# Performance work log

Hardware: AMD Instinct MI355X
Metric: run time of the kernel (lower is better)

## Reference

```python
import jax, jax.numpy as jnp
import numpy as np

DEPTH, HEADS, K, EPS = 4, 8, 3, 1e-5
DIM, CIN, COUT = 128, 64, 64


def conv1x1(x, w, b=None):
    y = jnp.einsum('oi,bihw->bohw', w, x)
    return y if b is None else y + b[None, :, None, None]


def dilated_conv3x3(x, w, b, d):
    y = jax.lax.conv_general_dilated(
        x, w, window_strides=(1, 1), padding=[(d, d), (d, d)],
        rhs_dilation=(d, d), dimension_numbers=('NCHW', 'OIHW', 'NCHW'))
    return y + b[None, :, None, None]


def batchnorm_train(x, g, b):
    # BatchNorm2d in training mode: biased batch stats over (B,H,W)
    mu = jnp.mean(x, axis=(0, 2, 3), keepdims=True)
    var = jnp.var(x, axis=(0, 2, 3), keepdims=True)
    return (x - mu) * jax.lax.rsqrt(var + EPS) * g[None, :, None, None] + b[None, :, None, None]


def unfold3(x):
    # nn.Unfold(k=3, pad=1): (B,C,H,W) -> (B,C,k*k,H,W), patch index row-major (dy,dx)
    B, C, H, W = x.shape
    p = K // 2
    xp = jnp.pad(x, ((0, 0), (0, 0), (p, p), (p, p)))
    return jnp.stack([xp[:, :, dy:dy + H, dx:dx + W]
                      for dy in range(K) for dx in range(K)], axis=2)


def local_self_attention(x, qkv_w, fc_w, fc_b):
    B, C, H, W = x.shape
    c = C // HEADS
    scale = c ** -0.5
    qkv = conv1x1(x, qkv_w)                      # (B,3C,H,W)
    q, k, v = jnp.split(qkv, 3, axis=1)
    shape6 = lambda t: unfold3(t).reshape(B, HEADS, c, K * K, H, W)
    q, k, v = shape6(q) * scale, shape6(k), shape6(v)
    # NOTE: original einsum labels dim2 (channels/head) as n/m and dim3 (k^2) as the
    # contracted axis, i.e. channel-attention contracted over the 9 patch positions.
    dots = jnp.einsum('bhnkij,bhmkij->bhnmij', q, k)   # (B,h,c,c,H,W)
    attn = jax.nn.softmax(dots, axis=3)
    out = jnp.einsum('bhnmij,bhmkij->bhnkij', attn, v)  # (B,h,c,k^2,H,W)
    out = out.reshape(B, C, K * K, H, W).sum(axis=2)
    return conv1x1(out, fc_w, fc_b) + x


def setup_inputs() -> dict:
    key = jax.random.key(0)
    ks = jax.random.split(key, 12)
    s = 0.05
    return {
        'x': jax.random.normal(ks[0], (2, CIN, 96, 96), jnp.float32),
        'w_in': jax.random.normal(ks[1], (DIM, CIN), jnp.float32) * s,
        'b_in': jnp.zeros((DIM,), jnp.float32),
        'conv_w': jax.random.normal(ks[2], (DEPTH, DIM, DIM, 3, 3), jnp.float32) * s,
        'conv_b': jnp.zeros((DEPTH, DIM), jnp.float32),
        'bn_g': jnp.ones((DEPTH, DIM), jnp.float32),
        'bn_b': jnp.zeros((DEPTH, DIM), jnp.float32),
        'qkv_w': jax.random.normal(ks[3], (DEPTH, 3 * DIM, DIM), jnp.float32) * s,
        'fc_w': jax.random.normal(ks[4], (DEPTH, DIM, DIM), jnp.float32) * s,
        'fc_b': jnp.zeros((DEPTH, DIM), jnp.float32),
        'w_out': jax.random.normal(ks[5], (COUT, DIM), jnp.float32) * s,
        'b_out': jnp.zeros((COUT,), jnp.float32),
    }


def reference(x, w_in, b_in, conv_w, conv_b, bn_g, bn_b, qkv_w, fc_w, fc_b, w_out, b_out):
    h = conv1x1(x, w_in, b_in)
    for i in range(DEPTH):
        d = 2 ** i
        h = jax.nn.relu(batchnorm_train(dilated_conv3x3(h, conv_w[i], conv_b[i], d), bn_g[i], bn_b[i]))
        h = local_self_attention(h, qkv_w[i], fc_w[i], fc_b[i])
    return conv1x1(h, w_out, b_out)
```

## Files before the change

### kernel.cpp

```cpp
#include <hip/hip_runtime.h>
#include <math.h>

typedef __attribute__((ext_vector_type(8))) short bf16x8;
typedef __attribute__((ext_vector_type(4))) float f32x4;
typedef __attribute__((ext_vector_type(4))) unsigned short us4;
typedef __attribute__((ext_vector_type(8))) unsigned short us8;

constexpr int BB = 2;
constexpr int CC = 128;
constexpr int HH = 96, WW = 96;
constexpr int PP = HH * WW;
constexpr int NN = BB * PP;
constexpr size_t PLANE_F = (size_t)NN * CC;

__device__ __forceinline__ float bf2f(unsigned short u) {
    return __uint_as_float(((unsigned)u) << 16);
}
__device__ __forceinline__ unsigned short f2bf(float f) {
    unsigned u = __float_as_uint(f);
    unsigned r = u + 0x7fff + ((u >> 16) & 1);
    return (unsigned short)(r >> 16);
}

__global__ __launch_bounds__(256)
void k_wconv(const float* __restrict__ conv_w, const float* __restrict__ qkv_w,
             const float* __restrict__ fc_w, const float* __restrict__ w_in,
             const float* __restrict__ w_out,
             unsigned short* __restrict__ wcv, unsigned short* __restrict__ wqkv,
             unsigned short* __restrict__ wfc, unsigned short* __restrict__ wi,
             unsigned short* __restrict__ wo)
{
    int gid = blockIdx.x * 256 + threadIdx.x;
    if (gid < 589824) {
        int L = gid / 147456, r = gid % 147456;
        int o = r / 1152, k = r % 1152;
        int t = k / 128, c = k % 128;
        float v = conv_w[(((size_t)(L * 128 + o) * 128 + c) * 9) + t];
        wcv[gid] = f2bf(v);
    } else if (gid < 786432) {
        int g = gid - 589824;
        int o = (g % 49152) / 128;
        float v = qkv_w[g] * (o < 128 ? 0.25f : 1.0f);
        wqkv[g] = f2bf(v);
    } else if (gid < 851968) {
        int g = gid - 786432;
        wfc[g] = f2bf(fc_w[g]);
    } else if (gid < 860160) {
        int g = gid - 851968;
        wi[g] = f2bf(w_in[g]);
    } else if (gid < 868352) {
        int g = gid - 860160;
        wo[g] = f2bf(w_out[g]);
    }
}

__global__ __launch_bounds__(256)
void k_xconv(const float* __restrict__ x, unsigned short* __restrict__ xT)
{
    int n = blockIdx.x * 256 + threadIdx.x;
    int b = n / PP, p = n - b * PP;
    unsigned short* dst = xT + (size_t)n * 64;
    #pragma unroll
    for (int cg = 0; cg < 16; ++cg) {
        us4 st;
        #pragma unroll
        for (int r = 0; r < 4; ++r)
            st[r] = f2bf(x[((size_t)(b * 64 + cg * 4 + r)) * PP + p]);
        *reinterpret_cast<us4*>(dst + cg * 4) = st;
    }
}

template<int WM, int WN, int MODE, int DIL>
__global__ __launch_bounds__(WM * WN * 64)
void k_gemm(const unsigned short* __restrict__ W,
            const unsigned short* __restrict__ act,
            const float* __restrict__ bias,
            const unsigned short* __restrict__ resid,
            void* __restrict__ outp,
            const unsigned short* __restrict__ zp,
            int Kw, int Cin, int Cout)
{
    int tid = threadIdx.x;
    int lane = tid & 63, wv = tid >> 6;
    int wm = wv % WM, wn = wv / WM;
    int l15 = lane & 15, kg = lane >> 4;

    int n_base = blockIdx.x * (WN * 96) + wn * 96;
    int o_base = blockIdx.y * (WM * 64) + wm * 64;

    const unsigned short* wbase[4];
    #pragma unroll
    for (int fm = 0; fm < 4; ++fm) {
        int o = o_base + fm * 16 + l15;
        wbase[fm] = W + (size_t)o * Kw + kg * 8;
    }

    const unsigned short* bbase[6];
    int iF[6], jF[6];
    #pragma unroll
    for (int fn = 0; fn < 6; ++fn) {
        int n = n_base + fn * 16 + l15;
        bbase[fn] = act + (size_t)n * Cin + kg * 8;
        if (DIL > 0) {
            int pix = n % PP;
            iF[fn] = pix / WW;
            jF[fn] = pix % WW;
        }
    }

    f32x4 acc[4][6];
    #pragma unroll
    for (int fm = 0; fm < 4; ++fm)
        #pragma unroll
        for (int fn = 0; fn < 6; ++fn)
            acc[fm][fn] = (f32x4){0.f, 0.f, 0.f, 0.f};

    if constexpr (DIL > 0) {
        const unsigned short* zpk = zp + kg * 8;
        int t0 = blockIdx.z * 3;
        for (int t = t0; t < t0 + 3; ++t) {
            int oy = (t / 3 - 1) * DIL, ox = (t % 3 - 1) * DIL;
            int disp = (oy * WW + ox) * Cin;
            const unsigned short* baddr[6];
            #pragma unroll
            for (int fn = 0; fn < 6; ++fn) {
                bool v = ((unsigned)(iF[fn] + oy) < (unsigned)HH) &&
                         ((unsigned)(jF[fn] + ox) < (unsigned)WW);
                baddr[fn] = v ? (bbase[fn] + disp) : zpk;
            }
            #pragma unroll
            for (int c0 = 0; c0 < 128; c0 += 32) {
                bf16x8 a[4], b[6];
                #pragma unroll
                for (int fm = 0; fm < 4; ++fm)
                    a[fm] = *reinterpret_cast<const bf16x8*>(wbase[fm] + t * 128 + c0);
                #pragma unroll
                for (int fn = 0; fn < 6; ++fn)
                    b[fn] = *reinterpret_cast<const bf16x8*>(baddr[fn] + c0);
                #pragma unroll
                for (int fm = 0; fm < 4; ++fm)
                    #pragma unroll
                    for (int fn = 0; fn < 6; ++fn)
                        acc[fm][fn] = __builtin_amdgcn_mfma_f32_16x16x32_bf16(
                            a[fm], b[fn], acc[fm][fn], 0, 0, 0);
            }
        }
    } else {
        #pragma unroll
        for (int k0 = 0; k0 < 128; k0 += 32) {
            if (k0 >= Cin) break;
            bf16x8 a[4], b[6];
            #pragma unroll
            for (int fm = 0; fm < 4; ++fm)
                a[fm] = *reinterpret_cast<const bf16x8*>(wbase[fm] + k0);
            #pragma unroll
            for (int fn = 0; fn < 6; ++fn)
                b[fn] = *reinterpret_cast<const bf16x8*>(bbase[fn] + k0);
            #pragma unroll
            for (int fm = 0; fm < 4; ++fm)
                #pragma unroll
                for (int fn = 0; fn < 6; ++fn)
                    acc[fm][fn] = __builtin_amdgcn_mfma_f32_16x16x32_bf16(
                        a[fm], b[fn], acc[fm][fn], 0, 0, 0);
        }
    }

    #pragma unroll
    for (int fm = 0; fm < 4; ++fm) {
        #pragma unroll
        for (int fn = 0; fn < 6; ++fn) {
            f32x4 v = acc[fm][fn];
            int n = n_base + fn * 16 + l15;
            int o0 = o_base + fm * 16 + kg * 4;
            if constexpr (MODE == 1) {
                float* op = (float*)outp + (size_t)blockIdx.z * PLANE_F;
                *reinterpret_cast<f32x4*>(op + (size_t)n * Cout + o0) = v;
            } else if constexpr (MODE == 0 || MODE == 2) {
                if (bias) {
                    #pragma unroll
                    for (int r = 0; r < 4; ++r) v[r] += bias[o0 + r];
                }
                if constexpr (MODE == 2) {
                    us4 rv = *reinterpret_cast<const us4*>(resid + (size_t)n * Cout + o0);
                    #pragma unroll
                    for (int r = 0; r < 4; ++r) v[r] += bf2f(rv[r]);
                }
                us4 st;
                #pragma unroll
                for (int r = 0; r < 4; ++r) st[r] = f2bf(v[r]);
                *reinterpret_cast<us4*>((unsigned short*)outp + (size_t)n * Cout + o0) = st;
            } else {
                int b_ = n / PP, p = n - b_ * PP;
                float* op = (float*)outp;
                #pragma unroll
                for (int r = 0; r < 4; ++r)
                    op[((size_t)(b_ * Cout + o0 + r)) * PP + p] = v[r] + bias[o0 + r];
            }
        }
    }
}

__global__ __launch_bounds__(256)
void k_bnpart(const float* __restrict__ y, float* __restrict__ partials)
{
    int t = threadIdx.x;
    int cq = t & 31, ng = t >> 5;
    int n0 = blockIdx.x * 384 + ng * 48;
    f32x4 s = {0.f, 0.f, 0.f, 0.f}, s2 = {0.f, 0.f, 0.f, 0.f};
    for (int r = 0; r < 48; ++r) {
        size_t idx = (size_t)(n0 + r) * CC + cq * 4;
        f32x4 a = *reinterpret_cast<const f32x4*>(y + idx);
        f32x4 b = *reinterpret_cast<const f32x4*>(y + PLANE_F + idx);
        f32x4 c = *reinterpret_cast<const f32x4*>(y + 2 * PLANE_F + idx);
        #pragma unroll
        for (int e = 0; e < 4; ++e) {
            float v = a[e] + b[e] + c[e];
            s[e] += v; s2[e] += v * v;
        }
    }
    __shared__ f32x4 ls[256], ls2[256];
    ls[t] = s; ls2[t] = s2;
    __syncthreads();
    if (t < 32) {
        f32x4 S = ls[t], S2 = ls2[t];
        #pragma unroll
        for (int g = 1; g < 8; ++g) {
            f32x4 a = ls[g * 32 + t], b = ls2[g * 32 + t];
            #pragma unroll
            for (int e = 0; e < 4; ++e) { S[e] += a[e]; S2[e] += b[e]; }
        }
        float* base = partials + (size_t)blockIdx.x * 256;
        *reinterpret_cast<f32x4*>(base + t * 4) = S;
        *reinterpret_cast<f32x4*>(base + 128 + t * 4) = S2;
    }
}

__global__ __launch_bounds__(128)
void k_bnfin(const float* __restrict__ partials, const float* __restrict__ g,
             const float* __restrict__ b, float* __restrict__ scsh)
{
    int c = threadIdx.x;
    float S = 0.f, S2 = 0.f;
    for (int blk = 0; blk < 48; ++blk) {
        S  += partials[(size_t)blk * 256 + c];
        S2 += partials[(size_t)blk * 256 + 128 + c];
    }
    const float inv = 1.f / (float)NN;
    float mu = S * inv;
    float var = S2 * inv - mu * mu;
    float sc = g[c] * rsqrtf(var + 1e-5f);
    scsh[c] = sc;
    scsh[128 + c] = b[c] - mu * sc;
}

__global__ __launch_bounds__(256)
void k_bnrelu(const float* __restrict__ y, const float* __restrict__ scsh,
              unsigned short* __restrict__ h)
{
    int gid = blockIdx.x * 256 + threadIdx.x;
    int c0 = (gid * 4) & 127;
    size_t idx = (size_t)gid * 4;
    f32x4 a = *reinterpret_cast<const f32x4*>(y + idx);
    f32x4 b = *reinterpret_cast<const f32x4*>(y + PLANE_F + idx);
    f32x4 c = *reinterpret_cast<const f32x4*>(y + 2 * PLANE_F + idx);
    us4 st;
    #pragma unroll
    for (int r = 0; r < 4; ++r) {
        float v = a[r] + b[r] + c[r];
        float f = fmaxf(fmaf(v, scsh[c0 + r], scsh[128 + c0 + r]), 0.f);
        st[r] = f2bf(f);
    }
    *reinterpret_cast<us4*>(h + idx) = st;
}

__global__ __launch_bounds__(256)
void k_attn(const unsigned short* __restrict__ qkv, unsigned short* __restrict__ att)
{
    int gid = blockIdx.x * 256 + threadIdx.x;
    int ng   = gid & 3;
    int head = (gid >> 2) & 7;
    int n    = gid >> 5;
    int pix = n % PP;
    int i = pix / WW, j = pix % WW;
    int hc = head * 16;
    const unsigned short* base = qkv + (size_t)n * 384;

    float dots[4][16];
    float vs[16];
    #pragma unroll
    for (int m = 0; m < 16; ++m) vs[m] = 0.f;
    #pragma unroll
    for (int nn = 0; nn < 4; ++nn)
        #pragma unroll
        for (int m = 0; m < 16; ++m) dots[nn][m] = 0.f;

    #pragma unroll
    for (int dy = 0; dy < 3; ++dy) {
        #pragma unroll
        for (int dx = 0; dx < 3; ++dx) {
            if (!(((unsigned)(i + dy - 1) < (unsigned)HH) &&
                  ((unsigned)(j + dx - 1) < (unsigned)WW))) continue;
            const unsigned short* pb = base + ((dy - 1) * WW + (dx - 1)) * 384;
            us4 q4 = *reinterpret_cast<const us4*>(pb + hc + ng * 4);
            us8 k0 = *reinterpret_cast<const us8*>(pb + 128 + hc);
            us8 k1 = *reinterpret_cast<const us8*>(pb + 128 + hc + 8);
            us8 v0 = *reinterpret_cast<const us8*>(pb + 256 + hc);
            us8 v1 = *reinterpret_cast<const us8*>(pb + 256 + hc + 8);
            float kf[16];
            #pragma unroll
            for (int e = 0; e < 8; ++e) {
                kf[e] = bf2f(k0[e]);
                kf[8 + e] = bf2f(k1[e]);
                vs[e] += bf2f(v0[e]);
                vs[8 + e] += bf2f(v1[e]);
            }
            #pragma unroll
            for (int nn = 0; nn < 4; ++nn) {
                float qf = bf2f(q4[nn]);
                #pragma unroll
                for (int m = 0; m < 16; ++m)
                    dots[nn][m] = fmaf(qf, kf[m], dots[nn][m]);
            }
        }
    }

    us4 st;
    #pragma unroll
    for (int nn = 0; nn < 4; ++nn) {
        float mx = dots[nn][0];
        #pragma unroll
        for (int m = 1; m < 16; ++m) mx = fmaxf(mx, dots[nn][m]);
        float den = 0.f, o = 0.f;
        #pragma unroll
        for (int m = 0; m < 16; ++m) {
            float e = __expf(dots[nn][m] - mx);
            den += e;
            o = fmaf(e, vs[m], o);
        }
        st[nn] = f2bf(o / den);
    }
    *reinterpret_cast<us4*>(att + (size_t)n * CC + hc + ng * 4) = st;
}

extern "C" void kernel_launch(void* const* d_in, const int* in_sizes, int n_in,
                              void* d_out, int out_size, void* d_ws, size_t ws_size,
                              hipStream_t stream)
{
    const float* x      = (const float*)d_in[0];
    const float* w_in   = (const float*)d_in[1];
    const float* b_in   = (const float*)d_in[2];
    const float* conv_w = (const float*)d_in[3];
    const float* bn_g   = (const float*)d_in[5];
    const float* bn_b   = (const float*)d_in[6];
    const float* qkv_w  = (const float*)d_in[7];
    const float* fc_w   = (const float*)d_in[8];
    const float* fc_b   = (const float*)d_in[9];
    const float* w_out  = (const float*)d_in[10];
    const float* b_out  = (const float*)d_in[11];

    char* ws = (char*)d_ws;
    unsigned short* zp    = (unsigned short*)(ws);
    unsigned short* wcv   = (unsigned short*)(ws + 4096);
    unsigned short* wqkv  = (unsigned short*)(ws + 1183744);
    unsigned short* wfc   = (unsigned short*)(ws + 1576960);
    unsigned short* wi    = (unsigned short*)(ws + 1708032);
    unsigned short* wo    = (unsigned short*)(ws + 1724416);
    unsigned short* xT    = (unsigned short*)(ws + 1740800);
    unsigned short* bufA  = (unsigned short*)(ws + 4100096);
    float*          ybuf  = (float*)        (ws + 8818688);
    unsigned short* attb  = (unsigned short*)(ws + 8818688);
    unsigned short* qkvb  = (unsigned short*)(ws + 18255872);
    unsigned short* hbuf  = (unsigned short*)(ws + 37130240);
    float*          parts = (float*)        (ws + 41848832);
    float*          scsh  = (float*)        (ws + 41897984);

    hipMemsetAsync(zp, 0, 4096, stream);

    k_wconv<<<3392, 256, 0, stream>>>(conv_w, qkv_w, fc_w, w_in, w_out,
                                      wcv, wqkv, wfc, wi, wo);
    k_xconv<<<NN / 256, 256, 0, stream>>>(x, xT);

    k_gemm<1, 2, 0, 0><<<dim3(96, 2), 128, 0, stream>>>(
        wi, xT, b_in, nullptr, bufA, nullptr, 64, 64, 128);

    for (int L = 0; L < 4; ++L) {
        const unsigned short* wc = wcv + (size_t)L * 147456;
        switch (L) {
            case 0: k_gemm<2, 2, 1, 1><<<dim3(96, 1, 3), 256, 0, stream>>>(
                        wc, bufA, nullptr, nullptr, ybuf, zp, 1152, 128, 128); break;
            case 1: k_gemm<2, 2, 1, 2><<<dim3(96, 1, 3), 256, 0, stream>>>(
                        wc, bufA, nullptr, nullptr, ybuf, zp, 1152, 128, 128); break;
            case 2: k_gemm<2, 2, 1, 4><<<dim3(96, 1, 3), 256, 0, stream>>>(
                        wc, bufA, nullptr, nullptr, ybuf, zp, 1152, 128, 128); break;
            case 3: k_gemm<2, 2, 1, 8><<<dim3(96, 1, 3), 256, 0, stream>>>(
                        wc, bufA, nullptr, nullptr, ybuf, zp, 1152, 128, 128); break;
        }
        k_bnpart<<<48, 256, 0, stream>>>(ybuf, parts);
        k_bnfin<<<1, 128, 0, stream>>>(parts, bn_g + L * 128, bn_b + L * 128, scsh);
        k_bnrelu<<<2304, 256, 0, stream>>>(ybuf, scsh, hbuf);

        k_gemm<1, 2, 0, 0><<<dim3(96, 6), 128, 0, stream>>>(
            wqkv + (size_t)L * 49152, hbuf, nullptr, nullptr, qkvb, nullptr, 128, 128, 384);

        k_attn<<<2304, 256, 0, stream>>>(qkvb, attb);

        k_gemm<1, 2, 2, 0><<<dim3(96, 2), 128, 0, stream>>>(
            wfc + (size_t)L * 16384, attb, fc_b + L * 128, hbuf, bufA, nullptr, 128, 128, 128);
    }

    k_gemm<1, 4, 3, 0><<<dim3(48, 1), 256, 0, stream>>>(
        wo, bufA, b_out, nullptr, (float*)d_out, nullptr, 128, 128, 64);
}
```

Baseline: 562.0 us.

## Fuse dilated conv split-K reduction and BN partial stats into one conv kernel

```diff
diff --git a/kernel.cpp b/kernel.cpp
--- a/kernel.cpp
+++ b/kernel.cpp
@@ -11,7 +11,7 @@
 constexpr int HH = 96, WW = 96;
 constexpr int PP = HH * WW;
 constexpr int NN = BB * PP;
-constexpr size_t PLANE_F = (size_t)NN * CC;
+constexpr int CONV_BLKS = NN / 48;
 
 __device__ __forceinline__ float bf2f(unsigned short u) {
     return __uint_as_float(((unsigned)u) << 16);
@@ -70,14 +70,141 @@
     }
 }
 
-template<int WM, int WN, int MODE, int DIL>
+template<int DIL>
+__global__ __launch_bounds__(384)
+void k_conv(const unsigned short* __restrict__ W,
+            const unsigned short* __restrict__ act,
+            float* __restrict__ y,
+            float* __restrict__ parts,
+            const unsigned short* __restrict__ zp)
+{
+    int tid = threadIdx.x;
+    int lane = tid & 63, wv = tid >> 6;
+    int wm = wv & 1, wz = wv >> 1;
+    int l15 = lane & 15, kg = lane >> 4;
+
+    int n_base = blockIdx.x * 48;
+    int o_base = wm * 64;
+
+    const unsigned short* wbase[4];
+    #pragma unroll
+    for (int fm = 0; fm < 4; ++fm)
+        wbase[fm] = W + (size_t)(o_base + fm * 16 + l15) * 1152 + kg * 8;
+
+    const unsigned short* bbase[3];
+    int iF[3], jF[3];
+    #pragma unroll
+    for (int fn = 0; fn < 3; ++fn) {
+        int n = n_base + fn * 16 + l15;
+        bbase[fn] = act + (size_t)n * 128 + kg * 8;
+        int pix = n % PP;
+        iF[fn] = pix / WW;
+        jF[fn] = pix % WW;
+    }
+
+    f32x4 acc[4][3];
+    #pragma unroll
+    for (int fm = 0; fm < 4; ++fm)
+        #pragma unroll
+        for (int fn = 0; fn < 3; ++fn)
+            acc[fm][fn] = (f32x4){0.f, 0.f, 0.f, 0.f};
+
+    const unsigned short* zpk = zp + kg * 8;
+    int t0 = wz * 3;
+    #pragma unroll
+    for (int tt = 0; tt < 3; ++tt) {
+        int t = t0 + tt;
+        int oy = (t / 3 - 1) * DIL, ox = (t % 3 - 1) * DIL;
+        int disp = (oy * WW + ox) * 128;
+        const unsigned short* baddr[3];
+        #pragma unroll
+        for (int fn = 0; fn < 3; ++fn) {
+            bool v = ((unsigned)(iF[fn] + oy) < (unsigned)HH) &&
+                     ((unsigned)(jF[fn] + ox) < (unsigned)WW);
+            baddr[fn] = v ? (bbase[fn] + disp) : zpk;
+        }
+        #pragma unroll
+        for (int c0 = 0; c0 < 128; c0 += 32) {
+            bf16x8 a[4], b[3];
+            #pragma unroll
+            for (int fm = 0; fm < 4; ++fm)
+                a[fm] = *reinterpret_cast<const bf16x8*>(wbase[fm] + t * 128 + c0);
+            #pragma unroll
+            for (int fn = 0; fn < 3; ++fn)
+                b[fn] = *reinterpret_cast<const bf16x8*>(baddr[fn] + c0);
+            #pragma unroll
+            for (int fm = 0; fm < 4; ++fm)
+                #pragma unroll
+                for (int fn = 0; fn < 3; ++fn)
+                    acc[fm][fn] = __builtin_amdgcn_mfma_f32_16x16x32_bf16(
+                        a[fm], b[fn], acc[fm][fn], 0, 0, 0);
+        }
+    }
+
+    __shared__ float red[4][48][64];
+    if (wz) {
+        int s = wm * 2 + wz - 1;
+        #pragma unroll
+        for (int fm = 0; fm < 4; ++fm)
+            #pragma unroll
+            for (int fn = 0; fn < 3; ++fn)
+                #pragma unroll
+                for (int r = 0; r < 4; ++r)
+                    red[s][fm * 12 + fn * 4 + r][lane] = acc[fm][fn][r];
+    }
+    __syncthreads();
+    if (wz == 0) {
+        #pragma unroll
+        for (int fm = 0; fm < 4; ++fm)
+            #pragma unroll
+            for (int fn = 0; fn < 3; ++fn)
+                #pragma unroll
+                for (int r = 0; r < 4; ++r)
+                    acc[fm][fn][r] += red[wm * 2][fm * 12 + fn * 4 + r][lane] +
+                                      red[wm * 2 + 1][fm * 12 + fn * 4 + r][lane];
+
+        #pragma unroll
+        for (int fm = 0; fm < 4; ++fm) {
+            int o0 = o_base + fm * 16 + kg * 4;
+            #pragma unroll
+            for (int fn = 0; fn < 3; ++fn) {
+                int n = n_base + fn * 16 + l15;
+                *reinterpret_cast<f32x4*>(y + (size_t)n * 128 + o0) = acc[fm][fn];
+            }
+        }
+
+        #pragma unroll
+        for (int fm = 0; fm < 4; ++fm) {
+            #pragma unroll
+            for (int r = 0; r < 4; ++r) {
+                float s = 0.f, s2 = 0.f;
+                #pragma unroll
+                for (int fn = 0; fn < 3; ++fn) {
+                    float v = acc[fm][fn][r];
+                    s += v; s2 += v * v;
+                }
+                #pragma unroll
+                for (int m = 1; m <= 8; m <<= 1) {
+                    s  += __shfl_xor(s,  m, 64);
+                    s2 += __shfl_xor(s2, m, 64);
+                }
+                if (l15 == 0) {
+                    int c = o_base + fm * 16 + kg * 4 + r;
+                    parts[(size_t)blockIdx.x * 256 + c]       = s;
+                    parts[(size_t)blockIdx.x * 256 + 128 + c] = s2;
+                }
+            }
+        }
+    }
+}
+
+template<int WM, int WN, int MODE>
 __global__ __launch_bounds__(WM * WN * 64)
 void k_gemm(const unsigned short* __restrict__ W,
             const unsigned short* __restrict__ act,
             const float* __restrict__ bias,
             const unsigned short* __restrict__ resid,
             void* __restrict__ outp,
-            const unsigned short* __restrict__ zp,
             int Kw, int Cin, int Cout)
 {
     int tid = threadIdx.x;
@@ -96,16 +223,10 @@
     }
 
     const unsigned short* bbase[6];
-    int iF[6], jF[6];
     #pragma unroll
     for (int fn = 0; fn < 6; ++fn) {
         int n = n_base + fn * 16 + l15;
         bbase[fn] = act + (size_t)n * Cin + kg * 8;
-        if (DIL > 0) {
-            int pix = n % PP;
-            iF[fn] = pix / WW;
-            jF[fn] = pix % WW;
-        }
     }
 
     f32x4 acc[4][6];
@@ -115,54 +236,22 @@
         for (int fn = 0; fn < 6; ++fn)
             acc[fm][fn] = (f32x4){0.f, 0.f, 0.f, 0.f};
 
-    if constexpr (DIL > 0) {
-        const unsigned short* zpk = zp + kg * 8;
-        int t0 = blockIdx.z * 3;
-        for (int t = t0; t < t0 + 3; ++t) {
-            int oy = (t / 3 - 1) * DIL, ox = (t % 3 - 1) * DIL;
-            int disp = (oy * WW + ox) * Cin;
-            const unsigned short* baddr[6];
-            #pragma unroll
-            for (int fn = 0; fn < 6; ++fn) {
-                bool v = ((unsigned)(iF[fn] + oy) < (unsigned)HH) &&
-                         ((unsigned)(jF[fn] + ox) < (unsigned)WW);
-                baddr[fn] = v ? (bbase[fn] + disp) : zpk;
-            }
-            #pragma unroll
-            for (int c0 = 0; c0 < 128; c0 += 32) {
-                bf16x8 a[4], b[6];
-                #pragma unroll
-                for (int fm = 0; fm < 4; ++fm)
-                    a[fm] = *reinterpret_cast<const bf16x8*>(wbase[fm] + t * 128 + c0);
-                #pragma unroll
-                for (int fn = 0; fn < 6; ++fn)
-                    b[fn] = *reinterpret_cast<const bf16x8*>(baddr[fn] + c0);
-                #pragma unroll
-                for (int fm = 0; fm < 4; ++fm)
-                    #pragma unroll
-                    for (int fn = 0; fn < 6; ++fn)
-                        acc[fm][fn] = __builtin_amdgcn_mfma_f32_16x16x32_bf16(
-                            a[fm], b[fn], acc[fm][fn], 0, 0, 0);
-            }
-        }
-    } else {
-        #pragma unroll
-        for (int k0 = 0; k0 < 128; k0 += 32) {
-            if (k0 >= Cin) break;
-            bf16x8 a[4], b[6];
-            #pragma unroll
-            for (int fm = 0; fm < 4; ++fm)
-                a[fm] = *reinterpret_cast<const bf16x8*>(wbase[fm] + k0);
+    #pragma unroll
+    for (int k0 = 0; k0 < 128; k0 += 32) {
+        if (k0 >= Cin) break;
+        bf16x8 a[4], b[6];
+        #pragma unroll
+        for (int fm = 0; fm < 4; ++fm)
+            a[fm] = *reinterpret_cast<const bf16x8*>(wbase[fm] + k0);
+        #pragma unroll
+        for (int fn = 0; fn < 6; ++fn)
+            b[fn] = *reinterpret_cast<const bf16x8*>(bbase[fn] + k0);
+        #pragma unroll
+        for (int fm = 0; fm < 4; ++fm)
             #pragma unroll
             for (int fn = 0; fn < 6; ++fn)
-                b[fn] = *reinterpret_cast<const bf16x8*>(bbase[fn] + k0);
-            #pragma unroll
-            for (int fm = 0; fm < 4; ++fm)
-                #pragma unroll
-                for (int fn = 0; fn < 6; ++fn)
-                    acc[fm][fn] = __builtin_amdgcn_mfma_f32_16x16x32_bf16(
-                        a[fm], b[fn], acc[fm][fn], 0, 0, 0);
-        }
+                acc[fm][fn] = __builtin_amdgcn_mfma_f32_16x16x32_bf16(
+                    a[fm], b[fn], acc[fm][fn], 0, 0, 0);
     }
 
     #pragma unroll
@@ -172,10 +261,7 @@
             f32x4 v = acc[fm][fn];
             int n = n_base + fn * 16 + l15;
             int o0 = o_base + fm * 16 + kg * 4;
-            if constexpr (MODE == 1) {
-                float* op = (float*)outp + (size_t)blockIdx.z * PLANE_F;
-                *reinterpret_cast<f32x4*>(op + (size_t)n * Cout + o0) = v;
-            } else if constexpr (MODE == 0 || MODE == 2) {
+            if constexpr (MODE == 0 || MODE == 2) {
                 if (bias) {
                     #pragma unroll
                     for (int r = 0; r < 4; ++r) v[r] += bias[o0 + r];
@@ -200,48 +286,13 @@
     }
 }
 
-__global__ __launch_bounds__(256)
-void k_bnpart(const float* __restrict__ y, float* __restrict__ partials)
-{
-    int t = threadIdx.x;
-    int cq = t & 31, ng = t >> 5;
-    int n0 = blockIdx.x * 384 + ng * 48;
-    f32x4 s = {0.f, 0.f, 0.f, 0.f}, s2 = {0.f, 0.f, 0.f, 0.f};
-    for (int r = 0; r < 48; ++r) {
-        size_t idx = (size_t)(n0 + r) * CC + cq * 4;
-        f32x4 a = *reinterpret_cast<const f32x4*>(y + idx);
-        f32x4 b = *reinterpret_cast<const f32x4*>(y + PLANE_F + idx);
-        f32x4 c = *reinterpret_cast<const f32x4*>(y + 2 * PLANE_F + idx);
-        #pragma unroll
-        for (int e = 0; e < 4; ++e) {
-            float v = a[e] + b[e] + c[e];
-            s[e] += v; s2[e] += v * v;
-        }
-    }
-    __shared__ f32x4 ls[256], ls2[256];
-    ls[t] = s; ls2[t] = s2;
-    __syncthreads();
-    if (t < 32) {
-        f32x4 S = ls[t], S2 = ls2[t];
-        #pragma unroll
-        for (int g = 1; g < 8; ++g) {
-            f32x4 a = ls[g * 32 + t], b = ls2[g * 32 + t];
-            #pragma unroll
-            for (int e = 0; e < 4; ++e) { S[e] += a[e]; S2[e] += b[e]; }
-        }
-        float* base = partials + (size_t)blockIdx.x * 256;
-        *reinterpret_cast<f32x4*>(base + t * 4) = S;
-        *reinterpret_cast<f32x4*>(base + 128 + t * 4) = S2;
-    }
-}
-
 __global__ __launch_bounds__(128)
 void k_bnfin(const float* __restrict__ partials, const float* __restrict__ g,
-             const float* __restrict__ b, float* __restrict__ scsh)
+             const float* __restrict__ b, float* __restrict__ scsh, int nblk)
 {
     int c = threadIdx.x;
     float S = 0.f, S2 = 0.f;
-    for (int blk = 0; blk < 48; ++blk) {
+    for (int blk = 0; blk < nblk; ++blk) {
         S  += partials[(size_t)blk * 256 + c];
         S2 += partials[(size_t)blk * 256 + 128 + c];
     }
@@ -260,14 +311,11 @@
     int gid = blockIdx.x * 256 + threadIdx.x;
     int c0 = (gid * 4) & 127;
     size_t idx = (size_t)gid * 4;
-    f32x4 a = *reinterpret_cast<const f32x4*>(y + idx);
-    f32x4 b = *reinterpret_cast<const f32x4*>(y + PLANE_F + idx);
-    f32x4 c = *reinterpret_cast<const f32x4*>(y + 2 * PLANE_F + idx);
+    f32x4 v = *reinterpret_cast<const f32x4*>(y + idx);
     us4 st;
     #pragma unroll
     for (int r = 0; r < 4; ++r) {
-        float v = a[r] + b[r] + c[r];
-        float f = fmaxf(fmaf(v, scsh[c0 + r], scsh[128 + c0 + r]), 0.f);
+        float f = fmaxf(fmaf(v[r], scsh[c0 + r], scsh[128 + c0 + r]), 0.f);
         st[r] = f2bf(f);
     }
     *reinterpret_cast<us4*>(h + idx) = st;
@@ -368,11 +416,11 @@
     unsigned short* xT    = (unsigned short*)(ws + 1740800);
     unsigned short* bufA  = (unsigned short*)(ws + 4100096);
     float*          ybuf  = (float*)        (ws + 8818688);
-    unsigned short* attb  = (unsigned short*)(ws + 8818688);
-    unsigned short* qkvb  = (unsigned short*)(ws + 18255872);
-    unsigned short* hbuf  = (unsigned short*)(ws + 37130240);
+    unsigned short* hbuf  = (unsigned short*)(ws + 18255872);
+    unsigned short* qkvb  = (unsigned short*)(ws + 22974464);
+    unsigned short* attb  = (unsigned short*)(ws + 37130240);
     float*          parts = (float*)        (ws + 41848832);
-    float*          scsh  = (float*)        (ws + 41897984);
+    float*          scsh  = (float*)        (ws + 42242048);
 
     hipMemsetAsync(zp, 0, 4096, stream);
 
@@ -380,34 +428,29 @@
                                       wcv, wqkv, wfc, wi, wo);
     k_xconv<<<NN / 256, 256, 0, stream>>>(x, xT);
 
-    k_gemm<1, 2, 0, 0><<<dim3(96, 2), 128, 0, stream>>>(
-        wi, xT, b_in, nullptr, bufA, nullptr, 64, 64, 128);
+    k_gemm<1, 2, 0><<<dim3(96, 2), 128, 0, stream>>>(
+        wi, xT, b_in, nullptr, bufA, 64, 64, 128);
 
     for (int L = 0; L < 4; ++L) {
         const unsigned short* wc = wcv + (size_t)L * 147456;
         switch (L) {
-            case 0: k_gemm<2, 2, 1, 1><<<dim3(96, 1, 3), 256, 0, stream>>>(
-                        wc, bufA, nullptr, nullptr, ybuf, zp, 1152, 128, 128); break;
-            case 1: k_gemm<2, 2, 1, 2><<<dim3(96, 1, 3), 256, 0, stream>>>(
-                        wc, bufA, nullptr, nullptr, ybuf, zp, 1152, 128, 128); break;
-            case 2: k_gemm<2, 2, 1, 4><<<dim3(96, 1, 3), 256, 0, stream>>>(
-                        wc, bufA, nullptr, nullptr, ybuf, zp, 1152, 128, 128); break;
-            case 3: k_gemm<2, 2, 1, 8><<<dim3(96, 1, 3), 256, 0, stream>>>(
-                        wc, bufA, nullptr, nullptr, ybuf, zp, 1152, 128, 128); break;
-        }
-        k_bnpart<<<48, 256, 0, stream>>>(ybuf, parts);
-        k_bnfin<<<1, 128, 0, stream>>>(parts, bn_g + L * 128, bn_b + L * 128, scsh);
+            case 0: k_conv<1><<<CONV_BLKS, 384, 0, stream>>>(wc, bufA, ybuf, parts, zp); break;
+            case 1: k_conv<2><<<CONV_BLKS, 384, 0, stream>>>(wc, bufA, ybuf, parts, zp); break;
+            case 2: k_conv<4><<<CONV_BLKS, 384, 0, stream>>>(wc, bufA, ybuf, parts, zp); break;
+            case 3: k_conv<8><<<CONV_BLKS, 384, 0, stream>>>(wc, bufA, ybuf, parts, zp); break;
+        }
+        k_bnfin<<<1, 128, 0, stream>>>(parts, bn_g + L * 128, bn_b + L * 128, scsh, CONV_BLKS);
         k_bnrelu<<<2304, 256, 0, stream>>>(ybuf, scsh, hbuf);
 
-        k_gemm<1, 2, 0, 0><<<dim3(96, 6), 128, 0, stream>>>(
-            wqkv + (size_t)L * 49152, hbuf, nullptr, nullptr, qkvb, nullptr, 128, 128, 384);
+        k_gemm<1, 2, 0><<<dim3(96, 6), 128, 0, stream>>>(
+            wqkv + (size_t)L * 49152, hbuf, nullptr, nullptr, qkvb, 128, 128, 384);
 
         k_attn<<<2304, 256, 0, stream>>>(qkvb, attb);
 
-        k_gemm<1, 2, 2, 0><<<dim3(96, 2), 128, 0, stream>>>(
-            wfc + (size_t)L * 16384, attb, fc_b + L * 128, hbuf, bufA, nullptr, 128, 128, 128);
-    }
-
-    k_gemm<1, 4, 3, 0><<<dim3(48, 1), 256, 0, stream>>>(
-        wo, bufA, b_out, nullptr, (float*)d_out, nullptr, 128, 128, 64);
-}
+        k_gemm<1, 2, 2><<<dim3(96, 2), 128, 0, stream>>>(
+            wfc + (size_t)L * 16384, attb, fc_b + L * 128, hbuf, bufA, 128, 128, 128);
+    }
+
+    k_gemm<1, 2, 3><<<dim3(96, 1), 128, 0, stream>>>(
+        wo, bufA, b_out, nullptr, (float*)d_out, 128, 128, 64);
+}
```

New measurement: 840.4 us. 49.5% more time.
